# Performance work log

Hardware: AMD Instinct MI355X
Metric: run time of the kernel (lower is better)

## Reference

```python
import jax, jax.numpy as jnp
import numpy as np

EMBED_DIM = 1024

def setup_inputs() -> dict:
    key = jax.random.key(0)
    ks = jax.random.split(key, 7)
    D = EMBED_DIM
    x = jax.random.normal(ks[0], (4, 2048, D), dtype=jnp.float32)
    s = 1.0 / np.sqrt(D)
    Wq = jax.random.normal(ks[1], (D, D), dtype=jnp.float32) * s
    bq = jnp.zeros((D,), dtype=jnp.float32)
    Wk = jax.random.normal(ks[2], (D, D), dtype=jnp.float32) * s
    bk = jnp.zeros((D,), dtype=jnp.float32)
    Wv = jax.random.normal(ks[3], (D, D), dtype=jnp.float32) * s
    bv = jnp.zeros((D,), dtype=jnp.float32)
    return {"x": x, "Wq": Wq, "bq": bq, "Wk": Wk, "bk": bk, "Wv": Wv, "bv": bv}

def reference(x, Wq, bq, Wk, bk, Wv, bv):
    # x: [B,S,D]; torch Linear: x @ W.T + b -> here W is stored as [D_in, D_out]
    Q = jnp.einsum('bsd,de->bse', x, Wq) + bq
    K = jnp.einsum('bsd,de->bse', x, Wk) + bk
    V = jnp.einsum('bsd,de->bse', x, Wv) + bv
    scale = 1.0 / jnp.sqrt(jnp.asarray(x.shape[-1], dtype=x.dtype))
    scores = jnp.einsum('bqd,bkd->bqk', Q, K) * scale  # [B,S,S]
    probs = jax.nn.softmax(scores, axis=-1)
    # dropout is identity in eval mode
    return jnp.einsum('bqk,bkd->bqd', probs, V)
```

## Files before the change

kernel.cpp:

```cpp
#include <hip/hip_runtime.h>
#include <hip/hip_bf16.h>
#include <hip/hip_fp16.h>
#include <stdint.h>
#include <stddef.h>
#include <string.h>

#define D_EMB 1024
#define SEQ   2048
#define BATCH 4

typedef short bf16x8  __attribute__((ext_vector_type(8)));
typedef short short8  __attribute__((ext_vector_type(8)));
typedef float f32x4   __attribute__((ext_vector_type(4)));

#define AS1 __attribute__((address_space(1)))
#define AS3 __attribute__((address_space(3)))

static __device__ __forceinline__ void async_copy16(const void* g, void* l) {
  __builtin_amdgcn_global_load_lds((const AS1 void*)g, (AS3 void*)l, 16, 0, 0);
}


#define BAR     __builtin_amdgcn_s_barrier()
#define VMCNT4  asm volatile("s_waitcnt vmcnt(4)" ::: "memory")
#define VMCNT0  asm volatile("s_waitcnt vmcnt(0)" ::: "memory")

#define STAGE_A(buf, h, kt) do {                                              \
    const __hip_bfloat16* _g = gA + (size_t)((h) * 128) * lda + ((kt) << 6);  \
    char* _l = (char*)sA + (buf) * 32768 + (h) * 16384 + wave * 1024;         \
    async_copy16(_g, _l);                                                     \
    async_copy16(_g + (size_t)64 * lda, _l + 8192);                           \
  } while (0)
#define STAGE_B(buf, h, kt) do {                                              \
    const __hip_bfloat16* _g = gB + (size_t)((h) * 128) * ldb + ((kt) << 6);  \
    char* _l = (char*)sB + (buf) * 32768 + (h) * 16384 + wave * 1024;         \
    async_copy16(_g, _l);                                                     \
    async_copy16(_g + (size_t)64 * ldb, _l + 8192);                           \
  } while (0)

#define LOAD_A(aF, lbuf, h) do {                                              \
    const __hip_bfloat16* _b = (lbuf) + (wr * 128 + (h) * 64 + lr) * 64;      \
    _Pragma("unroll")                                                         \
    for (int _i = 0; _i < 4; _i++) {                                          \
      aF[_i][0] = *(const bf16x8*)&_b[_i * 1024 + pc0];                       \
      aF[_i][1] = *(const bf16x8*)&_b[_i * 1024 + pc1];                       \
    }                                                                         \
  } while (0)
#define LOAD_B(bF, lbuf, g) do {                                              \
    const __hip_bfloat16* _b = (lbuf) + (wc * 64 + (g) * 32 + lr) * 64;       \
    _Pragma("unroll")                                                         \
    for (int _j = 0; _j < 2; _j++) {                                          \
      bF[_j][0] = *(const bf16x8*)&_b[_j * 1024 + pc0];                       \
      bF[_j][1] = *(const bf16x8*)&_b[_j * 1024 + pc1];                       \
    }                                                                         \
  } while (0)

#define MFMA_Q(aF, bF, h, g) do {                                             \
    __builtin_amdgcn_s_setprio(1);                                            \
    _Pragma("unroll")                                                         \
    for (int _i = 0; _i < 4; _i++)                                            \
      _Pragma("unroll")                                                       \
      for (int _j = 0; _j < 2; _j++) {                                        \
        acc[(h) * 4 + _i][(g) * 2 + _j] =                                     \
          __builtin_amdgcn_mfma_f32_16x16x32_bf16(aF[_i][0], bF[_j][0],       \
              acc[(h) * 4 + _i][(g) * 2 + _j], 0, 0, 0);                      \
        acc[(h) * 4 + _i][(g) * 2 + _j] =                                     \
          __builtin_amdgcn_mfma_f32_16x16x32_bf16(aF[_i][1], bF[_j][1],       \
              acc[(h) * 4 + _i][(g) * 2 + _j], 0, 0, 0);                      \
      }                                                                       \
    __builtin_amdgcn_s_setprio(0);                                            \
  } while (0)

static __device__ __forceinline__ void gemm256(
    const __hip_bfloat16* __restrict__ A, int lda,
    const __hip_bfloat16* __restrict__ Bt, int ldb,
    int K, f32x4 (&acc)[8][4])
{
  __shared__ __hip_bfloat16 sA[2][128 * 64 * 2];
  __shared__ __hip_bfloat16 sB[2][128 * 64 * 2];

  const int t    = threadIdx.x;
  const int wave = t >> 6;
  const int lane = t & 63;
  const int quad = lane >> 4;
  const int lr   = lane & 15;
  const int wr   = wave >> 2;
  const int wc   = wave & 3;

  const int r0 = t >> 3;
  const int cs = (((t & 7) ^ (r0 & 7)) << 3);
  const __hip_bfloat16* gA = A  + (size_t)r0 * lda + cs;
  const __hip_bfloat16* gB = Bt + (size_t)r0 * ldb + cs;

  const int pc0 = ((quad)     ^ (lr & 7)) << 3;
  const int pc1 = ((quad + 4) ^ (lr & 7)) << 3;

  const __hip_bfloat16* const lA0 = sA[0];
  const __hip_bfloat16* const lA1 = sA[1];
  const __hip_bfloat16* const lB0 = sB[0];
  const __hip_bfloat16* const lB1 = sB[1];

  const int nt    = K >> 6;
  const int niter = nt >> 1;

  STAGE_A(0, 0, 0);
  STAGE_A(0, 1, 0);
  STAGE_B(0, 0, 0);
  STAGE_B(0, 1, 0);
  STAGE_A(1, 0, 1);
  STAGE_B(1, 1, 1);
  VMCNT4;
  BAR;

  bf16x8 aF[4][2], bFa[2][2], bFb[2][2];

  for (int j = 0; j < niter - 1; ++j) {
    const int tb = 2 * j + 1, tc = tb + 1, td = tb + 2;

    LOAD_A(aF, lA0, 0); LOAD_B(bFa, lB0, 0);
    STAGE_B(1, 0, tb);
    BAR; MFMA_Q(aF, bFa, 0, 0); BAR;

    LOAD_B(bFb, lB0, 1);
    STAGE_A(1, 1, tb);
    BAR; MFMA_Q(aF, bFb, 0, 1); BAR;

    LOAD_A(aF, lA0, 1);
    STAGE_A(0, 0, tc);
    BAR; MFMA_Q(aF, bFb, 1, 1); BAR;

    STAGE_B(0, 1, tc);
    VMCNT4;
    BAR; MFMA_Q(aF, bFa, 1, 0); BAR;

    LOAD_A(aF, lA1, 0); LOAD_B(bFa, lB1, 0);
    STAGE_B(0, 0, tc);
    BAR; MFMA_Q(aF, bFa, 0, 0); BAR;

    LOAD_B(bFb, lB1, 1);
    STAGE_A(0, 1, tc);
    BAR; MFMA_Q(aF, bFb, 0, 1); BAR;

    LOAD_A(aF, lA1, 1);
    STAGE_A(1, 0, td);
    BAR; MFMA_Q(aF, bFb, 1, 1); BAR;

    STAGE_B(1, 1, td);
    VMCNT4;
    BAR; MFMA_Q(aF, bFa, 1, 0); BAR;
  }

  {
    const int tb = nt - 1;
    LOAD_A(aF, lA0, 0); LOAD_B(bFa, lB0, 0);
    STAGE_B(1, 0, tb);
    BAR; MFMA_Q(aF, bFa, 0, 0); BAR;

    LOAD_B(bFb, lB0, 1);
    STAGE_A(1, 1, tb);
    BAR; MFMA_Q(aF, bFb, 0, 1); BAR;

    LOAD_A(aF, lA0, 1);
    BAR; MFMA_Q(aF, bFb, 1, 1); BAR;

    VMCNT0;
    BAR; MFMA_Q(aF, bFa, 1, 0); BAR;

    LOAD_A(aF, lA1, 0); LOAD_B(bFa, lB1, 0);
    BAR; MFMA_Q(aF, bFa, 0, 0); BAR;

    LOAD_B(bFb, lB1, 1);
    BAR; MFMA_Q(aF, bFb, 0, 1); BAR;

    LOAD_A(aF, lA1, 1);
    BAR; MFMA_Q(aF, bFb, 1, 1); BAR;

    MFMA_Q(aF, bFa, 1, 0);
  }
}

#define ZERO_ACC(acc)                         \
  {                                           \
    f32x4 _z = {0.f, 0.f, 0.f, 0.f};          \
    _Pragma("unroll")                         \
    for (int _i = 0; _i < 8; _i++)            \
      _Pragma("unroll")                       \
      for (int _j = 0; _j < 4; _j++)          \
        acc[_i][_j] = _z;                     \
  }

__global__ __launch_bounds__(256) void prep_kernel(
    const float* __restrict__ x,
    const float* __restrict__ Wq,
    const float* __restrict__ Wk,
    const float* __restrict__ Wv,
    __hip_bfloat16* __restrict__ xb,
    __hip_bfloat16* __restrict__ Wt3)
{
  const int tx = threadIdx.x, ty = threadIdx.y;
  if (blockIdx.z == 3) {
    const int tid = ty * 32 + tx;
    const size_t base = ((size_t)blockIdx.y * 32 + blockIdx.x) * 8192;
#pragma unroll
    for (int p = 0; p < 8; p++) {
      const size_t i = base + p * 1024 + tid * 4;
      const float4 v = *(const float4*)(x + i);
      __hip_bfloat16 o[4] = {__float2bfloat16(v.x), __float2bfloat16(v.y),
                             __float2bfloat16(v.z), __float2bfloat16(v.w)};
      *(uint64_t*)(xb + i) = *(uint64_t*)o;
    }
    return;
  }
  const float* src = (blockIdx.z == 0) ? Wq : (blockIdx.z == 1) ? Wk : Wv;
  __hip_bfloat16* dst = Wt3 + (size_t)blockIdx.z * D_EMB * D_EMB;
  __shared__ __hip_bfloat16 tile[32][33];
  const int x0 = blockIdx.x * 32;
  const int y0 = blockIdx.y * 32;
#pragma unroll
  for (int i = 0; i < 32; i += 8)
    tile[ty + i][tx] = __float2bfloat16(src[(size_t)(y0 + ty + i) * D_EMB + (x0 + tx)]);
  __syncthreads();
#pragma unroll
  for (int i = 0; i < 32; i += 8)
    dst[(size_t)(x0 + ty + i) * D_EMB + (y0 + tx)] = tile[tx][ty + i];
}

__global__ __launch_bounds__(512, 2) void qkv_kernel(
    const __hip_bfloat16* __restrict__ xb,
    const __hip_bfloat16* __restrict__ Wt3,
    const float* __restrict__ bq,
    const float* __restrict__ bk,
    const float* __restrict__ bv,
    __hip_bfloat16* __restrict__ Q,
    __hip_bfloat16* __restrict__ Kb,
    __hip_bfloat16* __restrict__ Vt)
{
  const int mat = blockIdx.z;
  const int m0  = blockIdx.x * 256;
  const int n0  = blockIdx.y * 256;

  f32x4 acc[8][4];
  ZERO_ACC(acc);

  gemm256(xb + (size_t)m0 * D_EMB, D_EMB,
          Wt3 + (size_t)mat * D_EMB * D_EMB + (size_t)n0 * D_EMB, D_EMB,
          D_EMB, acc);

  const float* bias = (mat == 0) ? bq : (mat == 1) ? bk : bv;

  const int t = threadIdx.x;
  const int wave = t >> 6, lane = t & 63;
  const int quad = lane >> 4, lr = lane & 15;
  const int wr = wave >> 2, wc = wave & 3;

#pragma unroll
  for (int i = 0; i < 8; i++) {
#pragma unroll
    for (int j = 0; j < 4; j++) {
      const int n = n0 + wc * 64 + j * 16 + lr;
      const float bb = bias[n];
      const int mbase = m0 + wr * 128 + i * 16 + quad * 4;
      if (mat == 2) {
        const int b = mbase >> 11, s = mbase & 2047;
        __hip_bfloat16 pk[4];
#pragma unroll
        for (int r = 0; r < 4; r++) pk[r] = __float2bfloat16(acc[i][j][r] + bb);
        *(uint64_t*)&Vt[(size_t)b * D_EMB * SEQ + (size_t)n * SEQ + s] = *(uint64_t*)pk;
      } else {
        __hip_bfloat16* dst = (mat == 0) ? Q : Kb;
#pragma unroll
        for (int r = 0; r < 4; r++)
          dst[(size_t)(mbase + r) * D_EMB + n] = __float2bfloat16(acc[i][j][r] + bb);
      }
    }
  }
}

__global__ __launch_bounds__(512, 2) void scores_kernel(
    const __hip_bfloat16* __restrict__ Q,
    const __hip_bfloat16* __restrict__ Kb,
    __half* __restrict__ Sc)
{
  const int b  = blockIdx.z;
  const int m0 = blockIdx.y * 256;
  const int n0 = blockIdx.x * 256;

  f32x4 acc[8][4];
  ZERO_ACC(acc);

  gemm256(Q  + (size_t)b * SEQ * D_EMB + (size_t)m0 * D_EMB, D_EMB,
          Kb + (size_t)b * SEQ * D_EMB + (size_t)n0 * D_EMB, D_EMB,
          D_EMB, acc);

  __half* out = Sc + (size_t)b * SEQ * SEQ;
  const float scale = 0.03125f;

  const int t = threadIdx.x;
  const int wave = t >> 6, lane = t & 63;
  const int quad = lane >> 4, lr = lane & 15;
  const int wr = wave >> 2, wc = wave & 3;

#pragma unroll
  for (int i = 0; i < 8; i++)
#pragma unroll
    for (int j = 0; j < 4; j++) {
      const int n = n0 + wc * 64 + j * 16 + lr;
#pragma unroll
      for (int r = 0; r < 4; r++) {
        const int m = m0 + wr * 128 + i * 16 + quad * 4 + r;
        out[(size_t)m * SEQ + n] = __float2half(acc[i][j][r] * scale);
      }
    }
}

__global__ __launch_bounds__(256) void softmax_kernel(
    const __half* __restrict__ Sc, __hip_bfloat16* __restrict__ P)
{
  const int row = blockIdx.x;
  const __half* src = Sc + (size_t)row * SEQ;
  const int t = threadIdx.x;
  const int wave = t >> 6, lane = t & 63;

  const short8 raw = *(const short8*)(src + t * 8);
  float v[8];
#pragma unroll
  for (int i = 0; i < 8; i++) {
    const short si = raw[i];
    __half h;
    memcpy(&h, &si, sizeof(h));
    v[i] = __half2float(h);
  }

  float m = v[0];
#pragma unroll
  for (int i = 1; i < 8; i++) m = fmaxf(m, v[i]);
#pragma unroll
  for (int o = 32; o > 0; o >>= 1) m = fmaxf(m, __shfl_xor(m, o));

  __shared__ float redm[4];
  __shared__ float reds[4];
  if (lane == 0) redm[wave] = m;
  __syncthreads();
  m = fmaxf(fmaxf(redm[0], redm[1]), fmaxf(redm[2], redm[3]));

  float e[8], s = 0.f;
#pragma unroll
  for (int i = 0; i < 8; i++) { e[i] = __expf(v[i] - m); s += e[i]; }
#pragma unroll
  for (int o = 32; o > 0; o >>= 1) s += __shfl_xor(s, o);
  if (lane == 0) reds[wave] = s;
  __syncthreads();
  s = reds[0] + reds[1] + reds[2] + reds[3];

  const float inv = 1.f / s;
  short8 outp;
#pragma unroll
  for (int i = 0; i < 8; i++) {
    const __hip_bfloat16 b = __float2bfloat16(e[i] * inv);
    short sb;
    memcpy(&sb, &b, sizeof(sb));
    outp[i] = sb;
  }
  *(short8*)(P + (size_t)row * SEQ + t * 8) = outp;
}

__global__ __launch_bounds__(512, 2) void pv_kernel(
    const __hip_bfloat16* __restrict__ P,
    const __hip_bfloat16* __restrict__ Vt,
    float* __restrict__ out)
{
  const int b  = blockIdx.z;
  const int m0 = blockIdx.y * 256;
  const int n0 = blockIdx.x * 256;

  f32x4 acc[8][4];
  ZERO_ACC(acc);

  gemm256(P  + (size_t)b * SEQ * SEQ   + (size_t)m0 * SEQ, SEQ,
          Vt + (size_t)b * D_EMB * SEQ + (size_t)n0 * SEQ, SEQ,
          SEQ, acc);

  float* o = out + (size_t)b * SEQ * D_EMB;

  const int t = threadIdx.x;
  const int wave = t >> 6, lane = t & 63;
  const int quad = lane >> 4, lr = lane & 15;
  const int wr = wave >> 2, wc = wave & 3;

#pragma unroll
  for (int i = 0; i < 8; i++)
#pragma unroll
    for (int j = 0; j < 4; j++) {
      const int n = n0 + wc * 64 + j * 16 + lr;
#pragma unroll
      for (int r = 0; r < 4; r++) {
        const int m = m0 + wr * 128 + i * 16 + quad * 4 + r;
        o[(size_t)m * D_EMB + n] = acc[i][j][r];
      }
    }
}

extern "C" void kernel_launch(void* const* d_in, const int* in_sizes, int n_in,
                              void* d_out, int out_size, void* d_ws, size_t ws_size,
                              hipStream_t stream) {
  const float* x  = (const float*)d_in[0];
  const float* Wq = (const float*)d_in[1];
  const float* bq = (const float*)d_in[2];
  const float* Wk = (const float*)d_in[3];
  const float* bk = (const float*)d_in[4];
  const float* Wv = (const float*)d_in[5];
  const float* bv = (const float*)d_in[6];
  float* out = (float*)d_out;

  char* ws = (char*)d_ws;
  __hip_bfloat16* xb  = (__hip_bfloat16*)(ws);
  __hip_bfloat16* Wt3 = (__hip_bfloat16*)(ws + 16777216);
  __hip_bfloat16* Q   = (__hip_bfloat16*)(ws + 23068672);
  __hip_bfloat16* Kb  = (__hip_bfloat16*)(ws + 39845888);
  __hip_bfloat16* Vt  = (__hip_bfloat16*)(ws + 56623104);
  __half*         Sc  = (__half*)        (ws + 73400320);
  __hip_bfloat16* P   = (__hip_bfloat16*)(ws + 140509184);

  prep_kernel  <<<dim3(32, 32, 4), dim3(32, 8), 0, stream>>>(x, Wq, Wk, Wv, xb, Wt3);
  qkv_kernel   <<<dim3(32, 4, 3),  512,        0, stream>>>(xb, Wt3, bq, bk, bv, Q, Kb, Vt);
  scores_kernel<<<dim3(8, 8, 4),   512,        0, stream>>>(Q, Kb, Sc);
  softmax_kernel<<<dim3(8192),     256,        0, stream>>>(Sc, P);
  pv_kernel    <<<dim3(4, 8, 4),   512,        0, stream>>>(P, Vt, out);
}
```

Before: 270.9 us.

## Make each QKV block compute two output column tiles in one continuous pipeline

The QKV projection kernel now has each block handle two 256-wide output column tiles (col and col+6) back to back. The async-copy pipeline runs through 32 k-steps without draining, storing the first tile midway and zeroing the accumulators. This halves the grid to 192 blocks and is meant to amortise pipeline prologue and epilogue cost and reuse the x tile's L2 locality. The trade-off is fewer blocks, which may leave CUs idle, and a long unrolled body that raises register pressure.

```diff
diff --git a/kernel.cpp b/kernel.cpp
--- a/kernel.cpp
+++ b/kernel.cpp
@@ -36,6 +36,13 @@
     char* _l = (char*)sB + (buf) * 32768 + (h) * 16384 + wave * 1024;         \
     async_copy16(_g, _l);                                                     \
     async_copy16(_g + (size_t)64 * ldb, _l + 8192);                           \
+  } while (0)
+
+#define STAGE_P(dst, buf, h, gbase, kc) do {                                   \
+    const __hip_bfloat16* _g = (gbase) + (size_t)((h) * 128) * D_EMB + (kc);   \
+    char* _l = (char*)(dst) + (buf) * 32768 + (h) * 16384 + wave * 1024;       \
+    async_copy16(_g, _l);                                                      \
+    async_copy16(_g + (size_t)64 * D_EMB, _l + 8192);                          \
   } while (0)
 
 #define LOAD_A(aF, lbuf, h) do {                                              \
@@ -71,6 +78,16 @@
     __builtin_amdgcn_s_setprio(0);                                            \
   } while (0)
 
+#define ZERO_ACC(acc)                         \
+  {                                           \
+    f32x4 _z = {0.f, 0.f, 0.f, 0.f};          \
+    _Pragma("unroll")                         \
+    for (int _i = 0; _i < 8; _i++)            \
+      _Pragma("unroll")                       \
+      for (int _j = 0; _j < 4; _j++)          \
+        acc[_i][_j] = _z;                     \
+  }
+
 static __device__ __forceinline__ void gemm256(
     const __hip_bfloat16* __restrict__ A, int lda,
     const __hip_bfloat16* __restrict__ Bt, int ldb,
@@ -179,16 +196,6 @@
   }
 }
 
-#define ZERO_ACC(acc)                         \
-  {                                           \
-    f32x4 _z = {0.f, 0.f, 0.f, 0.f};          \
-    _Pragma("unroll")                         \
-    for (int _i = 0; _i < 8; _i++)            \
-      _Pragma("unroll")                       \
-      for (int _j = 0; _j < 4; _j++)          \
-        acc[_i][_j] = _z;                     \
-  }
-
 __global__ __launch_bounds__(256) void prep_kernel(
     const float* __restrict__ x,
     const float* __restrict__ Wq,
@@ -223,6 +230,42 @@
 #pragma unroll
   for (int i = 0; i < 32; i += 8)
     dst[(size_t)(x0 + ty + i) * D_EMB + (y0 + tx)] = tile[tx][ty + i];
+}
+
+static __device__ __forceinline__ void qkv_store(
+    f32x4 (&acc)[8][4], int col, int m0,
+    const float* __restrict__ bq, const float* __restrict__ bk,
+    const float* __restrict__ bv,
+    __hip_bfloat16* __restrict__ Q, __hip_bfloat16* __restrict__ Kb,
+    __hip_bfloat16* __restrict__ Vt, int t)
+{
+  const int mat = col >> 2;
+  const int n0  = (col & 3) << 8;
+  const float* bias = (mat == 0) ? bq : (mat == 1) ? bk : bv;
+  const int wave = t >> 6, lane = t & 63;
+  const int quad = lane >> 4, lr = lane & 15;
+  const int wr = wave >> 2, wc = wave & 3;
+#pragma unroll
+  for (int i = 0; i < 8; i++) {
+#pragma unroll
+    for (int j = 0; j < 4; j++) {
+      const int n = n0 + wc * 64 + j * 16 + lr;
+      const float bb = bias[n];
+      const int mbase = m0 + wr * 128 + i * 16 + quad * 4;
+      if (mat == 2) {
+        const int b = mbase >> 11, s = mbase & 2047;
+        __hip_bfloat16 pk[4];
+#pragma unroll
+        for (int r = 0; r < 4; r++) pk[r] = __float2bfloat16(acc[i][j][r] + bb);
+        *(uint64_t*)&Vt[(size_t)b * D_EMB * SEQ + (size_t)n * SEQ + s] = *(uint64_t*)pk;
+      } else {
+        __hip_bfloat16* dst = (mat == 0) ? Q : Kb;
+#pragma unroll
+        for (int r = 0; r < 4; r++)
+          dst[(size_t)(mbase + r) * D_EMB + n] = __float2bfloat16(acc[i][j][r] + bb);
+      }
+    }
+  }
 }
 
 __global__ __launch_bounds__(512, 2) void qkv_kernel(
@@ -235,45 +278,123 @@
     __hip_bfloat16* __restrict__ Kb,
     __hip_bfloat16* __restrict__ Vt)
 {
-  const int mat = blockIdx.z;
-  const int m0  = blockIdx.x * 256;
-  const int n0  = blockIdx.y * 256;
+  __shared__ __hip_bfloat16 sA[2][128 * 64 * 2];
+  __shared__ __hip_bfloat16 sB[2][128 * 64 * 2];
+
+  const int t    = threadIdx.x;
+  const int wave = t >> 6;
+  const int lane = t & 63;
+  const int quad = lane >> 4;
+  const int lr   = lane & 15;
+  const int wr   = wave >> 2;
+  const int wc   = wave & 3;
+
+  const int m0   = blockIdx.x * 256;
+  const int col0 = blockIdx.y;
+
+  const int r0 = t >> 3;
+  const int cs = (((t & 7) ^ (r0 & 7)) << 3);
+  const __hip_bfloat16* gA  = xb + (size_t)m0 * D_EMB + (size_t)r0 * D_EMB + cs;
+  const __hip_bfloat16* gB0 = Wt3 + ((size_t)col0 << 18) + (size_t)r0 * D_EMB + cs;
+  const __hip_bfloat16* gB1 = gB0 + ((size_t)6 << 18);
+
+  const int pc0 = ((quad)     ^ (lr & 7)) << 3;
+  const int pc1 = ((quad + 4) ^ (lr & 7)) << 3;
+
+  const __hip_bfloat16* const lA0 = sA[0];
+  const __hip_bfloat16* const lA1 = sA[1];
+  const __hip_bfloat16* const lB0 = sB[0];
+  const __hip_bfloat16* const lB1 = sB[1];
 
   f32x4 acc[8][4];
   ZERO_ACC(acc);
 
-  gemm256(xb + (size_t)m0 * D_EMB, D_EMB,
-          Wt3 + (size_t)mat * D_EMB * D_EMB + (size_t)n0 * D_EMB, D_EMB,
-          D_EMB, acc);
-
-  const float* bias = (mat == 0) ? bq : (mat == 1) ? bk : bv;
-
-  const int t = threadIdx.x;
-  const int wave = t >> 6, lane = t & 63;
-  const int quad = lane >> 4, lr = lane & 15;
-  const int wr = wave >> 2, wc = wave & 3;
-
-#pragma unroll
-  for (int i = 0; i < 8; i++) {
-#pragma unroll
-    for (int j = 0; j < 4; j++) {
-      const int n = n0 + wc * 64 + j * 16 + lr;
-      const float bb = bias[n];
-      const int mbase = m0 + wr * 128 + i * 16 + quad * 4;
-      if (mat == 2) {
-        const int b = mbase >> 11, s = mbase & 2047;
-        __hip_bfloat16 pk[4];
-#pragma unroll
-        for (int r = 0; r < 4; r++) pk[r] = __float2bfloat16(acc[i][j][r] + bb);
-        *(uint64_t*)&Vt[(size_t)b * D_EMB * SEQ + (size_t)n * SEQ + s] = *(uint64_t*)pk;
-      } else {
-        __hip_bfloat16* dst = (mat == 0) ? Q : Kb;
-#pragma unroll
-        for (int r = 0; r < 4; r++)
-          dst[(size_t)(mbase + r) * D_EMB + n] = __float2bfloat16(acc[i][j][r] + bb);
-      }
+  STAGE_P(sA, 0, 0, gA,  0);
+  STAGE_P(sA, 0, 1, gA,  0);
+  STAGE_P(sB, 0, 0, gB0, 0);
+  STAGE_P(sB, 0, 1, gB0, 0);
+  STAGE_P(sA, 1, 0, gA,  64);
+  STAGE_P(sB, 1, 1, gB0, 64);
+  VMCNT4;
+  BAR;
+
+  bf16x8 aF[4][2], bFa[2][2], bFb[2][2];
+
+  for (int j = 0; j < 15; ++j) {
+    const int tb = 2 * j + 1, tc = tb + 1, td = tb + 2;
+    const __hip_bfloat16* bTb = (tb & 16) ? gB1 : gB0;
+    const __hip_bfloat16* bTc = (tc & 16) ? gB1 : gB0;
+    const __hip_bfloat16* bTd = (td & 16) ? gB1 : gB0;
+    const int kb  = (tb & 15) << 6;
+    const int kc2 = (tc & 15) << 6;
+    const int kd  = (td & 15) << 6;
+
+    LOAD_A(aF, lA0, 0); LOAD_B(bFa, lB0, 0);
+    STAGE_P(sB, 1, 0, bTb, kb);
+    BAR; MFMA_Q(aF, bFa, 0, 0); BAR;
+
+    LOAD_B(bFb, lB0, 1);
+    STAGE_P(sA, 1, 1, gA, kb);
+    BAR; MFMA_Q(aF, bFb, 0, 1); BAR;
+
+    LOAD_A(aF, lA0, 1);
+    STAGE_P(sA, 0, 0, gA, kc2);
+    BAR; MFMA_Q(aF, bFb, 1, 1); BAR;
+
+    STAGE_P(sB, 0, 1, bTc, kc2);
+    VMCNT4;
+    BAR; MFMA_Q(aF, bFa, 1, 0); BAR;
+
+    LOAD_A(aF, lA1, 0); LOAD_B(bFa, lB1, 0);
+    STAGE_P(sB, 0, 0, bTc, kc2);
+    BAR; MFMA_Q(aF, bFa, 0, 0); BAR;
+
+    LOAD_B(bFb, lB1, 1);
+    STAGE_P(sA, 0, 1, gA, kc2);
+    BAR; MFMA_Q(aF, bFb, 0, 1); BAR;
+
+    LOAD_A(aF, lA1, 1);
+    STAGE_P(sA, 1, 0, gA, kd);
+    BAR; MFMA_Q(aF, bFb, 1, 1); BAR;
+
+    STAGE_P(sB, 1, 1, bTd, kd);
+    VMCNT4;
+    BAR; MFMA_Q(aF, bFa, 1, 0); BAR;
+
+    if (j == 7) {
+      qkv_store(acc, col0, m0, bq, bk, bv, Q, Kb, Vt, t);
+      ZERO_ACC(acc);
     }
   }
+
+  {
+    LOAD_A(aF, lA0, 0); LOAD_B(bFa, lB0, 0);
+    STAGE_P(sB, 1, 0, gB1, 15 << 6);
+    BAR; MFMA_Q(aF, bFa, 0, 0); BAR;
+
+    LOAD_B(bFb, lB0, 1);
+    STAGE_P(sA, 1, 1, gA, 15 << 6);
+    BAR; MFMA_Q(aF, bFb, 0, 1); BAR;
+
+    LOAD_A(aF, lA0, 1);
+    BAR; MFMA_Q(aF, bFb, 1, 1); BAR;
+
+    VMCNT0;
+    BAR; MFMA_Q(aF, bFa, 1, 0); BAR;
+
+    LOAD_A(aF, lA1, 0); LOAD_B(bFa, lB1, 0);
+    BAR; MFMA_Q(aF, bFa, 0, 0); BAR;
+
+    LOAD_B(bFb, lB1, 1);
+    BAR; MFMA_Q(aF, bFb, 0, 1); BAR;
+
+    LOAD_A(aF, lA1, 1);
+    BAR; MFMA_Q(aF, bFb, 1, 1); BAR;
+
+    MFMA_Q(aF, bFa, 1, 0);
+  }
+
+  qkv_store(acc, col0 + 6, m0, bq, bk, bv, Q, Kb, Vt, t);
 }
 
 __global__ __launch_bounds__(512, 2) void scores_kernel(
@@ -422,7 +543,7 @@
   __hip_bfloat16* P   = (__hip_bfloat16*)(ws + 140509184);
 
   prep_kernel  <<<dim3(32, 32, 4), dim3(32, 8), 0, stream>>>(x, Wq, Wk, Wv, xb, Wt3);
-  qkv_kernel   <<<dim3(32, 4, 3),  512,        0, stream>>>(xb, Wt3, bq, bk, bv, Q, Kb, Vt);
+  qkv_kernel   <<<dim3(32, 6, 1),  512,        0, stream>>>(xb, Wt3, bq, bk, bv, Q, Kb, Vt);
   scores_kernel<<<dim3(8, 8, 4),   512,        0, stream>>>(Q, Kb, Sc);
   softmax_kernel<<<dim3(8192),     256,        0, stream>>>(Sc, P);
   pv_kernel    <<<dim3(4, 8, 4),   512,        0, stream>>>(P, Vt, out);
```

Measured after the change: 303.2 us. 1.12x slower.

## Use 256x128 output tiles in PV GEMM to double block count

Applied to the files above, without the earlier changes.

Adds a gemm256x128 routine with a narrower B tile and halved accumulator set, and switches pv_kernel to it with a grid of 8x8x4 instead of 4x8x4. The intent is to fill more of the GPU's compute units, since 128 blocks of 256x256 leave many CUs idle on a 256-CU part. The cost is more reloading of the P matrix across column tiles and lower arithmetic intensity per block; the pipeline wait counts were retuned for the smaller B stage.

```diff
diff --git a/kernel.cpp b/kernel.cpp
--- a/kernel.cpp
+++ b/kernel.cpp
@@ -23,6 +23,7 @@
 
 #define BAR     __builtin_amdgcn_s_barrier()
 #define VMCNT4  asm volatile("s_waitcnt vmcnt(4)" ::: "memory")
+#define VMCNT3  asm volatile("s_waitcnt vmcnt(3)" ::: "memory")
 #define VMCNT0  asm volatile("s_waitcnt vmcnt(0)" ::: "memory")
 
 #define STAGE_A(buf, h, kt) do {                                              \
@@ -36,6 +37,11 @@
     char* _l = (char*)sB + (buf) * 32768 + (h) * 16384 + wave * 1024;         \
     async_copy16(_g, _l);                                                     \
     async_copy16(_g + (size_t)64 * ldb, _l + 8192);                           \
+  } while (0)
+#define STAGE_B1(buf, h, kt) do {                                             \
+    const __hip_bfloat16* _g = gB + (size_t)((h) * 64) * ldb + ((kt) << 6);   \
+    char* _l = (char*)sB + (buf) * 16384 + (h) * 8192 + wave * 1024;          \
+    async_copy16(_g, _l);                                                     \
   } while (0)
 
 #define LOAD_A(aF, lbuf, h) do {                                              \
@@ -53,6 +59,11 @@
       bF[_j][0] = *(const bf16x8*)&_b[_j * 1024 + pc0];                       \
       bF[_j][1] = *(const bf16x8*)&_b[_j * 1024 + pc1];                       \
     }                                                                         \
+  } while (0)
+#define LOAD_B1(bF, lbuf, g) do {                                             \
+    const __hip_bfloat16* _b = (lbuf) + (wc * 32 + (g) * 16 + lr) * 64;       \
+    bF[0] = *(const bf16x8*)&_b[pc0];                                         \
+    bF[1] = *(const bf16x8*)&_b[pc1];                                         \
   } while (0)
 
 #define MFMA_Q(aF, bF, h, g) do {                                             \
@@ -70,6 +81,38 @@
       }                                                                       \
     __builtin_amdgcn_s_setprio(0);                                            \
   } while (0)
+#define MFMA_Q1(aF, bF, h, g) do {                                            \
+    __builtin_amdgcn_s_setprio(1);                                            \
+    _Pragma("unroll")                                                         \
+    for (int _i = 0; _i < 4; _i++) {                                          \
+      acc[(h) * 4 + _i][(g)] =                                                \
+        __builtin_amdgcn_mfma_f32_16x16x32_bf16(aF[_i][0], bF[0],             \
+            acc[(h) * 4 + _i][(g)], 0, 0, 0);                                 \
+      acc[(h) * 4 + _i][(g)] =                                                \
+        __builtin_amdgcn_mfma_f32_16x16x32_bf16(aF[_i][1], bF[1],             \
+            acc[(h) * 4 + _i][(g)], 0, 0, 0);                                 \
+    }                                                                         \
+    __builtin_amdgcn_s_setprio(0);                                            \
+  } while (0)
+
+#define ZERO_ACC(acc)                         \
+  {                                           \
+    f32x4 _z = {0.f, 0.f, 0.f, 0.f};          \
+    _Pragma("unroll")                         \
+    for (int _i = 0; _i < 8; _i++)            \
+      _Pragma("unroll")                       \
+      for (int _j = 0; _j < 4; _j++)          \
+        acc[_i][_j] = _z;                     \
+  }
+#define ZERO_ACC2(acc)                        \
+  {                                           \
+    f32x4 _z = {0.f, 0.f, 0.f, 0.f};          \
+    _Pragma("unroll")                         \
+    for (int _i = 0; _i < 8; _i++)            \
+      _Pragma("unroll")                       \
+      for (int _j = 0; _j < 2; _j++)          \
+        acc[_i][_j] = _z;                     \
+  }
 
 static __device__ __forceinline__ void gemm256(
     const __hip_bfloat16* __restrict__ A, int lda,
@@ -179,15 +222,113 @@
   }
 }
 
-#define ZERO_ACC(acc)                         \
-  {                                           \
-    f32x4 _z = {0.f, 0.f, 0.f, 0.f};          \
-    _Pragma("unroll")                         \
-    for (int _i = 0; _i < 8; _i++)            \
-      _Pragma("unroll")                       \
-      for (int _j = 0; _j < 4; _j++)          \
-        acc[_i][_j] = _z;                     \
-  }
+static __device__ __forceinline__ void gemm256x128(
+    const __hip_bfloat16* __restrict__ A, int lda,
+    const __hip_bfloat16* __restrict__ Bt, int ldb,
+    int K, f32x4 (&acc)[8][2])
+{
+  __shared__ __hip_bfloat16 sA[2][128 * 64 * 2];
+  __shared__ __hip_bfloat16 sB[2][64 * 64 * 2];
+
+  const int t    = threadIdx.x;
+  const int wave = t >> 6;
+  const int lane = t & 63;
+  const int quad = lane >> 4;
+  const int lr   = lane & 15;
+  const int wr   = wave >> 2;
+  const int wc   = wave & 3;
+
+  const int r0 = t >> 3;
+  const int cs = (((t & 7) ^ (r0 & 7)) << 3);
+  const __hip_bfloat16* gA = A  + (size_t)r0 * lda + cs;
+  const __hip_bfloat16* gB = Bt + (size_t)r0 * ldb + cs;
+
+  const int pc0 = ((quad)     ^ (lr & 7)) << 3;
+  const int pc1 = ((quad + 4) ^ (lr & 7)) << 3;
+
+  const __hip_bfloat16* const lA0 = sA[0];
+  const __hip_bfloat16* const lA1 = sA[1];
+  const __hip_bfloat16* const lB0 = sB[0];
+  const __hip_bfloat16* const lB1 = sB[1];
+
+  const int nt    = K >> 6;
+  const int niter = nt >> 1;
+
+  STAGE_A(0, 0, 0);
+  STAGE_A(0, 1, 0);
+  STAGE_B1(0, 0, 0);
+  STAGE_B1(0, 1, 0);
+  STAGE_A(1, 0, 1);
+  STAGE_B1(1, 1, 1);
+  VMCNT3;
+  BAR;
+
+  bf16x8 aF[4][2], bFa[2], bFb[2];
+
+  for (int j = 0; j < niter - 1; ++j) {
+    const int tb = 2 * j + 1, tc = tb + 1, td = tb + 2;
+
+    LOAD_A(aF, lA0, 0); LOAD_B1(bFa, lB0, 0);
+    STAGE_B1(1, 0, tb);
+    BAR; MFMA_Q1(aF, bFa, 0, 0); BAR;
+
+    LOAD_B1(bFb, lB0, 1);
+    STAGE_A(1, 1, tb);
+    BAR; MFMA_Q1(aF, bFb, 0, 1); BAR;
+
+    LOAD_A(aF, lA0, 1);
+    STAGE_A(0, 0, tc);
+    BAR; MFMA_Q1(aF, bFb, 1, 1); BAR;
+
+    STAGE_B1(0, 1, tc);
+    VMCNT3;
+    BAR; MFMA_Q1(aF, bFa, 1, 0); BAR;
+
+    LOAD_A(aF, lA1, 0); LOAD_B1(bFa, lB1, 0);
+    STAGE_B1(0, 0, tc);
+    BAR; MFMA_Q1(aF, bFa, 0, 0); BAR;
+
+    LOAD_B1(bFb, lB1, 1);
+    STAGE_A(0, 1, tc);
+    BAR; MFMA_Q1(aF, bFb, 0, 1); BAR;
+
+    LOAD_A(aF, lA1, 1);
+    STAGE_A(1, 0, td);
+    BAR; MFMA_Q1(aF, bFb, 1, 1); BAR;
+
+    STAGE_B1(1, 1, td);
+    VMCNT3;
+    BAR; MFMA_Q1(aF, bFa, 1, 0); BAR;
+  }
+
+  {
+    const int tb = nt - 1;
+    LOAD_A(aF, lA0, 0); LOAD_B1(bFa, lB0, 0);
+    STAGE_B1(1, 0, tb);
+    BAR; MFMA_Q1(aF, bFa, 0, 0); BAR;
+
+    LOAD_B1(bFb, lB0, 1);
+    STAGE_A(1, 1, tb);
+    BAR; MFMA_Q1(aF, bFb, 0, 1); BAR;
+
+    LOAD_A(aF, lA0, 1);
+    BAR; MFMA_Q1(aF, bFb, 1, 1); BAR;
+
+    VMCNT0;
+    BAR; MFMA_Q1(aF, bFa, 1, 0); BAR;
+
+    LOAD_A(aF, lA1, 0); LOAD_B1(bFa, lB1, 0);
+    BAR; MFMA_Q1(aF, bFa, 0, 0); BAR;
+
+    LOAD_B1(bFb, lB1, 1);
+    BAR; MFMA_Q1(aF, bFb, 0, 1); BAR;
+
+    LOAD_A(aF, lA1, 1);
+    BAR; MFMA_Q1(aF, bFb, 1, 1); BAR;
+
+    MFMA_Q1(aF, bFa, 1, 0);
+  }
+}
 
 __global__ __launch_bounds__(256) void prep_kernel(
     const float* __restrict__ x,
@@ -371,14 +512,14 @@
 {
   const int b  = blockIdx.z;
   const int m0 = blockIdx.y * 256;
-  const int n0 = blockIdx.x * 256;
-
-  f32x4 acc[8][4];
-  ZERO_ACC(acc);
-
-  gemm256(P  + (size_t)b * SEQ * SEQ   + (size_t)m0 * SEQ, SEQ,
-          Vt + (size_t)b * D_EMB * SEQ + (size_t)n0 * SEQ, SEQ,
-          SEQ, acc);
+  const int n0 = blockIdx.x * 128;
+
+  f32x4 acc[8][2];
+  ZERO_ACC2(acc);
+
+  gemm256x128(P  + (size_t)b * SEQ * SEQ   + (size_t)m0 * SEQ, SEQ,
+              Vt + (size_t)b * D_EMB * SEQ + (size_t)n0 * SEQ, SEQ,
+              SEQ, acc);
 
   float* o = out + (size_t)b * SEQ * D_EMB;
 
@@ -390,8 +531,8 @@
 #pragma unroll
   for (int i = 0; i < 8; i++)
 #pragma unroll
-    for (int j = 0; j < 4; j++) {
-      const int n = n0 + wc * 64 + j * 16 + lr;
+    for (int j = 0; j < 2; j++) {
+      const int n = n0 + wc * 32 + j * 16 + lr;
 #pragma unroll
       for (int r = 0; r < 4; r++) {
         const int m = m0 + wr * 128 + i * 16 + quad * 4 + r;
@@ -425,5 +566,5 @@
   qkv_kernel   <<<dim3(32, 4, 3),  512,        0, stream>>>(xb, Wt3, bq, bk, bv, Q, Kb, Vt);
   scores_kernel<<<dim3(8, 8, 4),   512,        0, stream>>>(Q, Kb, Sc);
   softmax_kernel<<<dim3(8192),     256,        0, stream>>>(Sc, P);
-  pv_kernel    <<<dim3(4, 8, 4),   512,        0, stream>>>(P, Vt, out);
-}
+  pv_kernel    <<<dim3(8, 8, 4),   512,        0, stream>>>(P, Vt, out);
+}
```

Result: no change. 267.3 us (-1.3%).

## Fold Wq·Wk^T into one matrix, split-K the PV GEMM, retune load pipeline

Applied to the files above, without the earlier changes.

Precomputes M = Wq·Wk^T (and the bias term x·Wk·bq) so the scores become (x·M)·x^T plus a per-key column term. This drops the separate K projection, and the bk term is dropped because it is constant along each softmax row. The PV GEMM is split along K into two halves that accumulate into the output with atomic adds after a memset, doubling the block count to fill more CUs. The gemm256 staging order is also rearranged with a deeper vmcnt wait. The trade-offs are an extra 1024³ GEMM and prep work, possible precision loss from rounding M to bf16, and atomic and memset traffic on the output.

```diff
diff --git a/kernel.cpp b/kernel.cpp
--- a/kernel.cpp
+++ b/kernel.cpp
@@ -22,7 +22,7 @@
 
 
 #define BAR     __builtin_amdgcn_s_barrier()
-#define VMCNT4  asm volatile("s_waitcnt vmcnt(4)" ::: "memory")
+#define VMCNT6  asm volatile("s_waitcnt vmcnt(6)" ::: "memory")
 #define VMCNT0  asm volatile("s_waitcnt vmcnt(0)" ::: "memory")
 
 #define STAGE_A(buf, h, kt) do {                                              \
@@ -71,114 +71,6 @@
     __builtin_amdgcn_s_setprio(0);                                            \
   } while (0)
 
-static __device__ __forceinline__ void gemm256(
-    const __hip_bfloat16* __restrict__ A, int lda,
-    const __hip_bfloat16* __restrict__ Bt, int ldb,
-    int K, f32x4 (&acc)[8][4])
-{
-  __shared__ __hip_bfloat16 sA[2][128 * 64 * 2];
-  __shared__ __hip_bfloat16 sB[2][128 * 64 * 2];
-
-  const int t    = threadIdx.x;
-  const int wave = t >> 6;
-  const int lane = t & 63;
-  const int quad = lane >> 4;
-  const int lr   = lane & 15;
-  const int wr   = wave >> 2;
-  const int wc   = wave & 3;
-
-  const int r0 = t >> 3;
-  const int cs = (((t & 7) ^ (r0 & 7)) << 3);
-  const __hip_bfloat16* gA = A  + (size_t)r0 * lda + cs;
-  const __hip_bfloat16* gB = Bt + (size_t)r0 * ldb + cs;
-
-  const int pc0 = ((quad)     ^ (lr & 7)) << 3;
-  const int pc1 = ((quad + 4) ^ (lr & 7)) << 3;
-
-  const __hip_bfloat16* const lA0 = sA[0];
-  const __hip_bfloat16* const lA1 = sA[1];
-  const __hip_bfloat16* const lB0 = sB[0];
-  const __hip_bfloat16* const lB1 = sB[1];
-
-  const int nt    = K >> 6;
-  const int niter = nt >> 1;
-
-  STAGE_A(0, 0, 0);
-  STAGE_A(0, 1, 0);
-  STAGE_B(0, 0, 0);
-  STAGE_B(0, 1, 0);
-  STAGE_A(1, 0, 1);
-  STAGE_B(1, 1, 1);
-  VMCNT4;
-  BAR;
-
-  bf16x8 aF[4][2], bFa[2][2], bFb[2][2];
-
-  for (int j = 0; j < niter - 1; ++j) {
-    const int tb = 2 * j + 1, tc = tb + 1, td = tb + 2;
-
-    LOAD_A(aF, lA0, 0); LOAD_B(bFa, lB0, 0);
-    STAGE_B(1, 0, tb);
-    BAR; MFMA_Q(aF, bFa, 0, 0); BAR;
-
-    LOAD_B(bFb, lB0, 1);
-    STAGE_A(1, 1, tb);
-    BAR; MFMA_Q(aF, bFb, 0, 1); BAR;
-
-    LOAD_A(aF, lA0, 1);
-    STAGE_A(0, 0, tc);
-    BAR; MFMA_Q(aF, bFb, 1, 1); BAR;
-
-    STAGE_B(0, 1, tc);
-    VMCNT4;
-    BAR; MFMA_Q(aF, bFa, 1, 0); BAR;
-
-    LOAD_A(aF, lA1, 0); LOAD_B(bFa, lB1, 0);
-    STAGE_B(0, 0, tc);
-    BAR; MFMA_Q(aF, bFa, 0, 0); BAR;
-
-    LOAD_B(bFb, lB1, 1);
-    STAGE_A(0, 1, tc);
-    BAR; MFMA_Q(aF, bFb, 0, 1); BAR;
-
-    LOAD_A(aF, lA1, 1);
-    STAGE_A(1, 0, td);
-    BAR; MFMA_Q(aF, bFb, 1, 1); BAR;
-
-    STAGE_B(1, 1, td);
-    VMCNT4;
-    BAR; MFMA_Q(aF, bFa, 1, 0); BAR;
-  }
-
-  {
-    const int tb = nt - 1;
-    LOAD_A(aF, lA0, 0); LOAD_B(bFa, lB0, 0);
-    STAGE_B(1, 0, tb);
-    BAR; MFMA_Q(aF, bFa, 0, 0); BAR;
-
-    LOAD_B(bFb, lB0, 1);
-    STAGE_A(1, 1, tb);
-    BAR; MFMA_Q(aF, bFb, 0, 1); BAR;
-
-    LOAD_A(aF, lA0, 1);
-    BAR; MFMA_Q(aF, bFb, 1, 1); BAR;
-
-    VMCNT0;
-    BAR; MFMA_Q(aF, bFa, 1, 0); BAR;
-
-    LOAD_A(aF, lA1, 0); LOAD_B(bFa, lB1, 0);
-    BAR; MFMA_Q(aF, bFa, 0, 0); BAR;
-
-    LOAD_B(bFb, lB1, 1);
-    BAR; MFMA_Q(aF, bFb, 0, 1); BAR;
-
-    LOAD_A(aF, lA1, 1);
-    BAR; MFMA_Q(aF, bFb, 1, 1); BAR;
-
-    MFMA_Q(aF, bFa, 1, 0);
-  }
-}
-
 #define ZERO_ACC(acc)                         \
   {                                           \
     f32x4 _z = {0.f, 0.f, 0.f, 0.f};          \
@@ -189,17 +81,203 @@
         acc[_i][_j] = _z;                     \
   }
 
+static __device__ __forceinline__ void gemm256(
+    const __hip_bfloat16* __restrict__ A, int lda,
+    const __hip_bfloat16* __restrict__ Bt, int ldb,
+    int K, f32x4 (&acc)[8][4])
+{
+  __shared__ __hip_bfloat16 sA[2][128 * 64 * 2];
+  __shared__ __hip_bfloat16 sB[2][128 * 64 * 2];
+
+  const int t    = threadIdx.x;
+  const int wave = t >> 6;
+  const int lane = t & 63;
+  const int quad = lane >> 4;
+  const int lr   = lane & 15;
+  const int wr   = wave >> 2;
+  const int wc   = wave & 3;
+
+  const int r0 = t >> 3;
+  const int cs = (((t & 7) ^ (r0 & 7)) << 3);
+  const __hip_bfloat16* gA = A  + (size_t)r0 * lda + cs;
+  const __hip_bfloat16* gB = Bt + (size_t)r0 * ldb + cs;
+
+  const int pc0 = ((quad)     ^ (lr & 7)) << 3;
+  const int pc1 = ((quad + 4) ^ (lr & 7)) << 3;
+
+  const __hip_bfloat16* const lA0 = sA[0];
+  const __hip_bfloat16* const lA1 = sA[1];
+  const __hip_bfloat16* const lB0 = sB[0];
+  const __hip_bfloat16* const lB1 = sB[1];
+
+  const int nt    = K >> 6;
+  const int niter = nt >> 1;
+
+  STAGE_A(0, 0, 0);
+  STAGE_A(0, 1, 0);
+  STAGE_B(0, 0, 0);
+  STAGE_B(0, 1, 0);
+  STAGE_B(1, 0, 1);
+  STAGE_B(1, 1, 1);
+  STAGE_A(1, 0, 1);
+  VMCNT6;
+  BAR;
+
+  bf16x8 aF[4][2], bFa[2][2], bFb[2][2];
+
+  for (int j = 0; j < niter - 1; ++j) {
+    const int tb = 2 * j + 1, tc = tb + 1, td = tb + 2;
+
+    LOAD_A(aF, lA0, 0); LOAD_B(bFa, lB0, 0);
+    STAGE_A(1, 1, tb);
+    BAR; MFMA_Q(aF, bFa, 0, 0); BAR;
+
+    LOAD_B(bFb, lB0, 1);
+    BAR; MFMA_Q(aF, bFb, 0, 1); BAR;
+
+    LOAD_A(aF, lA0, 1);
+    STAGE_B(0, 0, tc);
+    BAR; MFMA_Q(aF, bFb, 1, 1); BAR;
+
+    STAGE_B(0, 1, tc);
+    STAGE_A(0, 0, tc);
+    VMCNT6;
+    BAR; MFMA_Q(aF, bFa, 1, 0); BAR;
+
+    LOAD_A(aF, lA1, 0); LOAD_B(bFa, lB1, 0);
+    STAGE_A(0, 1, tc);
+    BAR; MFMA_Q(aF, bFa, 0, 0); BAR;
+
+    LOAD_B(bFb, lB1, 1);
+    BAR; MFMA_Q(aF, bFb, 0, 1); BAR;
+
+    LOAD_A(aF, lA1, 1);
+    STAGE_B(1, 0, td);
+    BAR; MFMA_Q(aF, bFb, 1, 1); BAR;
+
+    STAGE_B(1, 1, td);
+    STAGE_A(1, 0, td);
+    VMCNT6;
+    BAR; MFMA_Q(aF, bFa, 1, 0); BAR;
+  }
+
+  {
+    const int tb = nt - 1;
+    LOAD_A(aF, lA0, 0); LOAD_B(bFa, lB0, 0);
+    STAGE_A(1, 1, tb);
+    BAR; MFMA_Q(aF, bFa, 0, 0); BAR;
+
+    LOAD_B(bFb, lB0, 1);
+    BAR; MFMA_Q(aF, bFb, 0, 1); BAR;
+
+    LOAD_A(aF, lA0, 1);
+    BAR; MFMA_Q(aF, bFb, 1, 1); BAR;
+
+    VMCNT0;
+    BAR; MFMA_Q(aF, bFa, 1, 0); BAR;
+
+    LOAD_A(aF, lA1, 0); LOAD_B(bFa, lB1, 0);
+    BAR; MFMA_Q(aF, bFa, 0, 0); BAR;
+
+    LOAD_B(bFb, lB1, 1);
+    BAR; MFMA_Q(aF, bFb, 0, 1); BAR;
+
+    LOAD_A(aF, lA1, 1);
+    BAR; MFMA_Q(aF, bFb, 1, 1); BAR;
+
+    MFMA_Q(aF, bFa, 1, 0);
+  }
+}
+
+static __device__ __forceinline__ void gemm128(
+    const __hip_bfloat16* __restrict__ A, int lda,
+    const __hip_bfloat16* __restrict__ Bt, int ldb,
+    int K, f32x4 (&acc)[4][4])
+{
+  __shared__ __hip_bfloat16 ldsA[2][128 * 64];
+  __shared__ __hip_bfloat16 ldsB[2][128 * 64];
+
+  const int t    = threadIdx.x;
+  const int wave = t >> 6;
+  const int lane = t & 63;
+  const int quad = lane >> 4;
+  const int lr   = lane & 15;
+  const int wr   = wave >> 1;
+  const int wc   = wave & 1;
+
+  const int r0 = t >> 3;
+  const int c0 = (((t & 7) ^ (r0 & 7)) * 8);
+
+  const __hip_bfloat16* gA = A  + (size_t)r0 * lda + c0;
+  const __hip_bfloat16* gB = Bt + (size_t)r0 * ldb + c0;
+
+  const int niter = K >> 6;
+
+  {
+    char* lA = (char*)ldsA[0] + wave * 1024;
+    char* lB = (char*)ldsB[0] + wave * 1024;
+#pragma unroll
+    for (int ch = 0; ch < 4; ch++) {
+      async_copy16(gA + (size_t)(32 * ch) * lda, lA + 4096 * ch);
+      async_copy16(gB + (size_t)(32 * ch) * ldb, lB + 4096 * ch);
+    }
+  }
+
+  int buf = 0;
+  for (int it = 0; it < niter; ++it) {
+    __syncthreads();
+
+    if (it + 1 < niter) {
+      const int k0 = (it + 1) << 6;
+      char* lA = (char*)ldsA[buf ^ 1] + wave * 1024;
+      char* lB = (char*)ldsB[buf ^ 1] + wave * 1024;
+#pragma unroll
+      for (int ch = 0; ch < 4; ch++) {
+        async_copy16(gA + k0 + (size_t)(32 * ch) * lda, lA + 4096 * ch);
+        async_copy16(gB + k0 + (size_t)(32 * ch) * ldb, lB + 4096 * ch);
+      }
+    }
+
+    const __hip_bfloat16* bA = ldsA[buf];
+    const __hip_bfloat16* bB = ldsB[buf];
+#pragma unroll
+    for (int kk = 0; kk < 64; kk += 32) {
+      bf16x8 aF[4], bF[4];
+      const int lc = (kk >> 3) + quad;
+      const int pc = (lc ^ (lr & 7)) * 8;
+#pragma unroll
+      for (int i = 0; i < 4; i++)
+        aF[i] = *(const bf16x8*)&bA[(wr * 64 + i * 16 + lr) * 64 + pc];
+#pragma unroll
+      for (int j = 0; j < 4; j++)
+        bF[j] = *(const bf16x8*)&bB[(wc * 64 + j * 16 + lr) * 64 + pc];
+
+#pragma unroll
+      for (int i = 0; i < 4; i++)
+#pragma unroll
+        for (int j = 0; j < 4; j++)
+          acc[i][j] = __builtin_amdgcn_mfma_f32_16x16x32_bf16(aF[i], bF[j], acc[i][j], 0, 0, 0);
+    }
+    buf ^= 1;
+  }
+}
+
 __global__ __launch_bounds__(256) void prep_kernel(
     const float* __restrict__ x,
     const float* __restrict__ Wq,
     const float* __restrict__ Wk,
     const float* __restrict__ Wv,
+    const float* __restrict__ bq,
     __hip_bfloat16* __restrict__ xb,
-    __hip_bfloat16* __restrict__ Wt3)
+    __hip_bfloat16* __restrict__ Wqb,
+    __hip_bfloat16* __restrict__ Wkb,
+    __hip_bfloat16* __restrict__ Wvt,
+    float* __restrict__ u)
 {
   const int tx = threadIdx.x, ty = threadIdx.y;
-  if (blockIdx.z == 3) {
-    const int tid = ty * 32 + tx;
+  const int tid = ty * 32 + tx;
+  const int z = blockIdx.z;
+  if (z == 3) {
     const size_t base = ((size_t)blockIdx.y * 32 + blockIdx.x) * 8192;
 #pragma unroll
     for (int p = 0; p < 8; p++) {
@@ -211,28 +289,107 @@
     }
     return;
   }
-  const float* src = (blockIdx.z == 0) ? Wq : (blockIdx.z == 1) ? Wk : Wv;
-  __hip_bfloat16* dst = Wt3 + (size_t)blockIdx.z * D_EMB * D_EMB;
+  if (z < 2) {
+    const float* src = (z == 0) ? Wq : Wk;
+    __hip_bfloat16* dst = (z == 0) ? Wqb : Wkb;
+    const size_t i = ((size_t)blockIdx.y * 32 + blockIdx.x) * 1024 + tid * 4;
+    const float4 v = *(const float4*)(src + i);
+    __hip_bfloat16 o[4] = {__float2bfloat16(v.x), __float2bfloat16(v.y),
+                           __float2bfloat16(v.z), __float2bfloat16(v.w)};
+    *(uint64_t*)(dst + i) = *(uint64_t*)o;
+    return;
+  }
+  if (z == 4) {
+    if (blockIdx.y != 0 || blockIdx.x >= 4) return;
+    const int d = blockIdx.x * 256 + tid;
+    const float* row = Wk + (size_t)d * D_EMB;
+    float s = 0.f;
+    for (int e = 0; e < D_EMB; e += 4) {
+      const float4 a = *(const float4*)(row + e);
+      const float4 b = *(const float4*)(bq + e);
+      s += a.x * b.x + a.y * b.y + a.z * b.z + a.w * b.w;
+    }
+    u[d] = s;
+    return;
+  }
   __shared__ __hip_bfloat16 tile[32][33];
   const int x0 = blockIdx.x * 32;
   const int y0 = blockIdx.y * 32;
 #pragma unroll
   for (int i = 0; i < 32; i += 8)
-    tile[ty + i][tx] = __float2bfloat16(src[(size_t)(y0 + ty + i) * D_EMB + (x0 + tx)]);
+    tile[ty + i][tx] = __float2bfloat16(Wv[(size_t)(y0 + ty + i) * D_EMB + (x0 + tx)]);
   __syncthreads();
 #pragma unroll
   for (int i = 0; i < 32; i += 8)
-    dst[(size_t)(x0 + ty + i) * D_EMB + (y0 + tx)] = tile[tx][ty + i];
+    Wvt[(size_t)(x0 + ty + i) * D_EMB + (y0 + tx)] = tile[tx][ty + i];
+}
+
+__global__ __launch_bounds__(256) void mtw_kernel(
+    const __hip_bfloat16* __restrict__ Wkb,
+    const __hip_bfloat16* __restrict__ Wqb,
+    const __hip_bfloat16* __restrict__ xb,
+    const float* __restrict__ u,
+    __hip_bfloat16* __restrict__ Mt,
+    float* __restrict__ w)
+{
+  const int t = threadIdx.x;
+  if (blockIdx.y == 8) {
+    __shared__ float su[1024];
+#pragma unroll
+    for (int i = 0; i < 4; i++) su[t + 256 * i] = u[t + 256 * i];
+    __syncthreads();
+    const int s0 = blockIdx.x * 1024;
+#pragma unroll
+    for (int rr = 0; rr < 4; rr++) {
+      const int s = s0 + rr * 256 + t;
+      const __hip_bfloat16* row = xb + (size_t)s * D_EMB;
+      float sum = 0.f;
+      for (int e = 0; e < D_EMB; e += 8) {
+        const short8 v = *(const short8*)(row + e);
+#pragma unroll
+        for (int i = 0; i < 8; i++) {
+          __hip_bfloat16 hb; const short sv = v[i]; memcpy(&hb, &sv, 2);
+          sum += __bfloat162float(hb) * su[e + i];
+        }
+      }
+      w[s] = sum;
+    }
+    return;
+  }
+  const int m0 = blockIdx.x * 128;
+  const int n0 = blockIdx.y * 128;
+  f32x4 acc[4][4];
+  {
+    f32x4 z4 = {0.f, 0.f, 0.f, 0.f};
+#pragma unroll
+    for (int i = 0; i < 4; i++)
+#pragma unroll
+      for (int j = 0; j < 4; j++) acc[i][j] = z4;
+  }
+  gemm128(Wkb + (size_t)m0 * D_EMB, D_EMB,
+          Wqb + (size_t)n0 * D_EMB, D_EMB, D_EMB, acc);
+
+  const int wave = t >> 6, lane = t & 63;
+  const int quad = lane >> 4, lr = lane & 15;
+  const int wr = wave >> 1, wc = wave & 1;
+#pragma unroll
+  for (int i = 0; i < 4; i++)
+#pragma unroll
+    for (int j = 0; j < 4; j++) {
+      const int n = n0 + wc * 64 + j * 16 + lr;
+      const int mb = m0 + wr * 64 + i * 16 + quad * 4;
+#pragma unroll
+      for (int r = 0; r < 4; r++)
+        Mt[(size_t)(mb + r) * D_EMB + n] = __float2bfloat16(acc[i][j][r]);
+    }
 }
 
 __global__ __launch_bounds__(512, 2) void qkv_kernel(
     const __hip_bfloat16* __restrict__ xb,
-    const __hip_bfloat16* __restrict__ Wt3,
-    const float* __restrict__ bq,
-    const float* __restrict__ bk,
+    const __hip_bfloat16* __restrict__ Mt,
+    const __hip_bfloat16* __restrict__ Wvt,
     const float* __restrict__ bv,
-    __hip_bfloat16* __restrict__ Q,
-    __hip_bfloat16* __restrict__ Kb,
+    __hip_bfloat16* __restrict__ Y,
     __hip_bfloat16* __restrict__ Vt)
 {
   const int mat = blockIdx.z;
@@ -242,11 +399,9 @@
   f32x4 acc[8][4];
   ZERO_ACC(acc);
 
+  const __hip_bfloat16* Bt = (mat == 0) ? Mt : Wvt;
   gemm256(xb + (size_t)m0 * D_EMB, D_EMB,
-          Wt3 + (size_t)mat * D_EMB * D_EMB + (size_t)n0 * D_EMB, D_EMB,
-          D_EMB, acc);
-
-  const float* bias = (mat == 0) ? bq : (mat == 1) ? bk : bv;
+          Bt + (size_t)n0 * D_EMB, D_EMB, D_EMB, acc);
 
   const int t = threadIdx.x;
   const int wave = t >> 6, lane = t & 63;
@@ -258,27 +413,27 @@
 #pragma unroll
     for (int j = 0; j < 4; j++) {
       const int n = n0 + wc * 64 + j * 16 + lr;
-      const float bb = bias[n];
       const int mbase = m0 + wr * 128 + i * 16 + quad * 4;
-      if (mat == 2) {
+      if (mat == 1) {
+        const float bb = bv[n];
         const int b = mbase >> 11, s = mbase & 2047;
         __hip_bfloat16 pk[4];
 #pragma unroll
         for (int r = 0; r < 4; r++) pk[r] = __float2bfloat16(acc[i][j][r] + bb);
         *(uint64_t*)&Vt[(size_t)b * D_EMB * SEQ + (size_t)n * SEQ + s] = *(uint64_t*)pk;
       } else {
-        __hip_bfloat16* dst = (mat == 0) ? Q : Kb;
 #pragma unroll
         for (int r = 0; r < 4; r++)
-          dst[(size_t)(mbase + r) * D_EMB + n] = __float2bfloat16(acc[i][j][r] + bb);
+          Y[(size_t)(mbase + r) * D_EMB + n] = __float2bfloat16(acc[i][j][r]);
       }
     }
   }
 }
 
 __global__ __launch_bounds__(512, 2) void scores_kernel(
-    const __hip_bfloat16* __restrict__ Q,
-    const __hip_bfloat16* __restrict__ Kb,
+    const __hip_bfloat16* __restrict__ Y,
+    const __hip_bfloat16* __restrict__ xb,
+    const float* __restrict__ w,
     __half* __restrict__ Sc)
 {
   const int b  = blockIdx.z;
@@ -288,8 +443,8 @@
   f32x4 acc[8][4];
   ZERO_ACC(acc);
 
-  gemm256(Q  + (size_t)b * SEQ * D_EMB + (size_t)m0 * D_EMB, D_EMB,
-          Kb + (size_t)b * SEQ * D_EMB + (size_t)n0 * D_EMB, D_EMB,
+  gemm256(Y  + ((size_t)b * SEQ + m0) * D_EMB, D_EMB,
+          xb + ((size_t)b * SEQ + n0) * D_EMB, D_EMB,
           D_EMB, acc);
 
   __half* out = Sc + (size_t)b * SEQ * SEQ;
@@ -305,10 +460,11 @@
 #pragma unroll
     for (int j = 0; j < 4; j++) {
       const int n = n0 + wc * 64 + j * 16 + lr;
+      const float wv = w[(size_t)b * SEQ + n];
 #pragma unroll
       for (int r = 0; r < 4; r++) {
         const int m = m0 + wr * 128 + i * 16 + quad * 4 + r;
-        out[(size_t)m * SEQ + n] = __float2half(acc[i][j][r] * scale);
+        out[(size_t)m * SEQ + n] = __float2half((acc[i][j][r] + wv) * scale);
       }
     }
 }
@@ -371,14 +527,15 @@
 {
   const int b  = blockIdx.z;
   const int m0 = blockIdx.y * 256;
-  const int n0 = blockIdx.x * 256;
+  const int n0 = (blockIdx.x & 3) * 256;
+  const int kh = (blockIdx.x >> 2) * 1024;
 
   f32x4 acc[8][4];
   ZERO_ACC(acc);
 
-  gemm256(P  + (size_t)b * SEQ * SEQ   + (size_t)m0 * SEQ, SEQ,
-          Vt + (size_t)b * D_EMB * SEQ + (size_t)n0 * SEQ, SEQ,
-          SEQ, acc);
+  gemm256(P  + (size_t)b * SEQ * SEQ   + (size_t)m0 * SEQ + kh, SEQ,
+          Vt + (size_t)b * D_EMB * SEQ + (size_t)n0 * SEQ + kh, SEQ,
+          1024, acc);
 
   float* o = out + (size_t)b * SEQ * D_EMB;
 
@@ -395,7 +552,7 @@
 #pragma unroll
       for (int r = 0; r < 4; r++) {
         const int m = m0 + wr * 128 + i * 16 + quad * 4 + r;
-        o[(size_t)m * D_EMB + n] = acc[i][j][r];
+        unsafeAtomicAdd(&o[(size_t)m * D_EMB + n], acc[i][j][r]);
       }
     }
 }
@@ -408,22 +565,30 @@
   const float* bq = (const float*)d_in[2];
   const float* Wk = (const float*)d_in[3];
   const float* bk = (const float*)d_in[4];
+  const float* bv = (const float*)d_in[6];
   const float* Wv = (const float*)d_in[5];
-  const float* bv = (const float*)d_in[6];
+  (void)bk;
   float* out = (float*)d_out;
 
   char* ws = (char*)d_ws;
   __hip_bfloat16* xb  = (__hip_bfloat16*)(ws);
-  __hip_bfloat16* Wt3 = (__hip_bfloat16*)(ws + 16777216);
-  __hip_bfloat16* Q   = (__hip_bfloat16*)(ws + 23068672);
-  __hip_bfloat16* Kb  = (__hip_bfloat16*)(ws + 39845888);
-  __hip_bfloat16* Vt  = (__hip_bfloat16*)(ws + 56623104);
-  __half*         Sc  = (__half*)        (ws + 73400320);
-  __hip_bfloat16* P   = (__hip_bfloat16*)(ws + 140509184);
-
-  prep_kernel  <<<dim3(32, 32, 4), dim3(32, 8), 0, stream>>>(x, Wq, Wk, Wv, xb, Wt3);
-  qkv_kernel   <<<dim3(32, 4, 3),  512,        0, stream>>>(xb, Wt3, bq, bk, bv, Q, Kb, Vt);
-  scores_kernel<<<dim3(8, 8, 4),   512,        0, stream>>>(Q, Kb, Sc);
+  __hip_bfloat16* Wqb = (__hip_bfloat16*)(ws + 16777216);
+  __hip_bfloat16* Wkb = (__hip_bfloat16*)(ws + 18874368);
+  __hip_bfloat16* Wvt = (__hip_bfloat16*)(ws + 20971520);
+  __hip_bfloat16* Mt  = (__hip_bfloat16*)(ws + 23068672);
+  float*          u   = (float*)         (ws + 25165824);
+  float*          w   = (float*)         (ws + 25169920);
+  __hip_bfloat16* Y   = (__hip_bfloat16*)(ws + 25202688);
+  __hip_bfloat16* Vt  = (__hip_bfloat16*)(ws + 41979904);
+  __half*         Sc  = (__half*)        (ws + 58757120);
+  __hip_bfloat16* P   = (__hip_bfloat16*)(ws + 92311552);
+
+  hipMemsetAsync(out, 0, (size_t)BATCH * SEQ * D_EMB * 4, stream);
+  prep_kernel  <<<dim3(32, 32, 5), dim3(32, 8), 0, stream>>>(x, Wq, Wk, Wv, bq,
+                                                             xb, Wqb, Wkb, Wvt, u);
+  mtw_kernel   <<<dim3(8, 9),      256,        0, stream>>>(Wkb, Wqb, xb, u, Mt, w);
+  qkv_kernel   <<<dim3(32, 4, 2),  512,        0, stream>>>(xb, Mt, Wvt, bv, Y, Vt);
+  scores_kernel<<<dim3(8, 8, 4),   512,        0, stream>>>(Y, xb, w, Sc);
   softmax_kernel<<<dim3(8192),     256,        0, stream>>>(Sc, P);
-  pv_kernel    <<<dim3(4, 8, 4),   512,        0, stream>>>(P, Vt, out);
-}
+  pv_kernel    <<<dim3(8, 8, 4),   512,        0, stream>>>(P, Vt, out);
+}
```

New measurement: 362.8 us. 33.9% more time.
